# Kernel tuning notes

Hardware: AMD Instinct MI355X
Metric: run time of the kernel (lower is better)

Reference implementation:

```python
import jax, jax.numpy as jnp
import numpy as np

N, E = 50000, 800000
IN_DIM, OUT_DIM, EDGE_DIM = 128, 128, 6
LN_EPS = 1e-5


def setup_inputs() -> dict:
    key = jax.random.key(0)
    ks = jax.random.split(key, 9)
    w = lambda k, sh: (jax.random.normal(k, sh, jnp.float32) * 0.05)
    return {
        "x": jax.random.normal(ks[0], (N, IN_DIM), jnp.float32),
        "edge_attr": jax.random.normal(ks[1], (E, EDGE_DIM), jnp.float32),
        "Wn": w(ks[2], (IN_DIM, OUT_DIM)),
        "bn": jnp.zeros((OUT_DIM,), jnp.float32),
        "We": w(ks[3], (EDGE_DIM, OUT_DIM)),
        "be": jnp.zeros((OUT_DIM,), jnp.float32),
        "Wm": w(ks[4], (2 * OUT_DIM, OUT_DIM)),
        "bm": jnp.zeros((OUT_DIM,), jnp.float32),
        "gamma": jnp.ones((OUT_DIM,), jnp.float32),
        "beta": jnp.zeros((OUT_DIM,), jnp.float32),
        "edge_index": jax.random.randint(ks[5], (2, E), 0, N, jnp.int32),
    }


def reference(x, edge_attr, Wn, bn, We, be, Wm, bm, gamma, beta, edge_index):
    row, col = edge_index[0], edge_index[1]
    x_t = x @ Wn + bn                                  # [N, D]
    e_t = edge_attr @ We + be                          # [E, D]
    msgs = jnp.concatenate([x_t[col], e_t], axis=-1)   # gather + concat [E, 2D]
    msgs = jax.nn.relu(msgs @ Wm + bm)                 # [E, D]
    agg = jax.ops.segment_sum(msgs, row, num_segments=N)            # scatter_add
    deg = jax.ops.segment_sum(jnp.ones((E,), jnp.float32), row, num_segments=N)
    out = agg / jnp.clip(deg, 1.0)[:, None] + x_t      # mean-normalize + residual
    mu = out.mean(axis=-1, keepdims=True)
    var = out.var(axis=-1, keepdims=True)
    return (out - mu) * jax.lax.rsqrt(var + LN_EPS) * gamma + beta
```

## Files before the change

kernel.cpp:

```cpp
#include <hip/hip_runtime.h>
#include <hip/hip_bf16.h>

#define D 128
#define EDGE_DIM 6
#define LN_EPS 1e-5f
#define HIST_BLOCKS 2048

typedef __attribute__((ext_vector_type(8))) short short8;
typedef __attribute__((ext_vector_type(4))) float f32x4;
typedef __attribute__((ext_vector_type(2))) float f32x2;

static __device__ __forceinline__ float bf_lo(unsigned u) { return __uint_as_float(u << 16); }
static __device__ __forceinline__ float bf_hi(unsigned u) { return __uint_as_float(u & 0xffff0000u); }
static __device__ __forceinline__ unsigned short f2bf(float f) {
    __hip_bfloat16 h = __float2bfloat16(f);
    return *reinterpret_cast<unsigned short*>(&h);
}
static __device__ __forceinline__ unsigned f2fp8(float f) {
    unsigned u;
    asm("v_cvt_pk_fp8_f32 %0, %1, %2" : "=v"(u) : "v"(f), "v"(0.0f));
    return u & 0xffu;
}
static __device__ __forceinline__ f32x2 cvt2_fp8v(unsigned w) {
    f32x2 r;
    asm("v_cvt_pk_f32_fp8 %0, %1" : "=v"(r) : "v"(w));
    return r;
}

__global__ __launch_bounds__(128)
void setup_all(const float* __restrict__ Wn, const float* __restrict__ bn,
               const float* __restrict__ We, const float* __restrict__ be,
               const float* __restrict__ Wm, const float* __restrict__ bm,
               const int* __restrict__ ei, int E,
               float* __restrict__ Wnm, float* __restrict__ bnm,
               float* __restrict__ Wc, float* __restrict__ bc,
               int* __restrict__ cnt) {
    const int b = blockIdx.x;
    const int d = threadIdx.x;
    if (b < 128) {
        float acc = 0.f;
#pragma unroll 8
        for (int j = 0; j < D; ++j)
            acc = fmaf(Wn[b * D + j], Wm[j * D + d], acc);
        Wnm[b * D + d] = acc;
    } else if (b == 128) {
        float acc = 0.f;
#pragma unroll 8
        for (int j = 0; j < D; ++j)
            acc = fmaf(bn[j], Wm[j * D + d], acc);
        bnm[d] = acc;
    } else if (b < 135) {
        const int k = b - 129;
        float acc = 0.f;
#pragma unroll 8
        for (int j = 0; j < D; ++j)
            acc = fmaf(We[k * D + j], Wm[(D + j) * D + d], acc);
        Wc[k * D + d] = acc;
    } else if (b == 135) {
        float acc = bm[d];
#pragma unroll 8
        for (int j = 0; j < D; ++j)
            acc = fmaf(be[j], Wm[(D + j) * D + d], acc);
        bc[d] = acc;
    } else {
        for (int i = (b - 136) * 128 + d; i < E; i += HIST_BLOCKS * 128)
            atomicAdd(&cnt[ei[i]], 1);
    }
}

__global__ __launch_bounds__(1024)
void scan_pack(const int* __restrict__ cnt, int* __restrict__ start,
               int* __restrict__ cur, int* __restrict__ cursor, int n, int nscan,
               const float* __restrict__ Wn, const float* __restrict__ Wnm,
               unsigned short* __restrict__ Wb) {
    const int tid = threadIdx.x;
    if ((int)blockIdx.x >= nscan) {
        const int idx = ((int)blockIdx.x - nscan) * 1024 + tid;
        if (idx < 4096) {
            const int lane = idx & 63;
            const int s = (idx >> 6) & 3;
            const int ct = (idx >> 8) & 7;
            const int mat = idx >> 11;
            const float* W = mat ? Wnm : Wn;
            const int col = ct * 16 + (lane & 15);
            const int k0 = (lane >> 4) * 8 + 32 * s;
            short8 v;
#pragma unroll
            for (int j = 0; j < 8; ++j)
                v[j] = (short)f2bf(W[(size_t)(k0 + j) * D + col]);
            *reinterpret_cast<short8*>(Wb + (size_t)idx * 8) = v;
        }
        return;
    }
    __shared__ int wsum[16];
    __shared__ int sbase;
    const int lane = tid & 63, wid = tid >> 6;
    const int i = blockIdx.x * 1024 + tid;
    const int v = (i < n) ? cnt[i] : 0;
    int x = v;
#pragma unroll
    for (int off = 1; off < 64; off <<= 1) {
        int t = __shfl_up(x, off);
        if (lane >= off) x += t;
    }
    if (lane == 63) wsum[wid] = x;
    __syncthreads();
    if (wid == 0) {
        int w = (lane < 16) ? wsum[lane] : 0;
#pragma unroll
        for (int off = 1; off < 16; off <<= 1) {
            int t = __shfl_up(w, off);
            if (lane >= off) w += t;
        }
        if (lane < 16) wsum[lane] = w;
    }
    __syncthreads();
    const int total = wsum[15];
    if (tid == 0) sbase = atomicAdd(cursor, total);
    __syncthreads();
    const int woff = (wid > 0) ? wsum[wid - 1] : 0;
    if (i < n) {
        const int sv = sbase + woff + x - v;
        start[i] = sv;
        cur[i] = sv;
    }
}

__global__ __launch_bounds__(256)
void scat_gemm(const int* __restrict__ ei, int E, const float* __restrict__ ea,
               int* __restrict__ cur, uint4* __restrict__ rec, int nscat,
               const float* __restrict__ x, const unsigned short* __restrict__ Wb,
               const float* __restrict__ bn, const float* __restrict__ bnm,
               unsigned short* __restrict__ xtb, unsigned char* __restrict__ hb,
               int nrows) {
    __shared__ unsigned sR[2048 * 3];
    const int tid = threadIdx.x;
    if ((int)blockIdx.x < nscat) {
        const int base = blockIdx.x * 2048;
        const int nrec = min(2048, E - base);
        const float2* ea2 = reinterpret_cast<const float2*>(ea);
        for (int i = tid; i < nrec * 3; i += 256) {
            float2 p = ea2[(size_t)base * 3 + i];
            sR[i] = (unsigned)f2bf(p.x) | ((unsigned)f2bf(p.y) << 16);
        }
        __syncthreads();
        int rows[8], cols[8], pos[8];
#pragma unroll
        for (int it = 0; it < 8; ++it) {
            const int e = base + it * 256 + tid;
            const bool val = e < E;
            rows[it] = val ? ei[e] : -1;
            cols[it] = val ? ei[E + e] : 0;
        }
#pragma unroll
        for (int it = 0; it < 8; ++it)
            if (rows[it] >= 0) pos[it] = atomicAdd(&cur[rows[it]], 1);
#pragma unroll
        for (int it = 0; it < 8; ++it)
            if (rows[it] >= 0) {
                const int le = (it * 256 + tid) * 3;
                rec[pos[it]] = make_uint4((unsigned)cols[it], sR[le], sR[le + 1], sR[le + 2]);
            }
        return;
    }
    const int ntile = (nrows + 15) / 16;
    const int lane = tid & 63;
    const int wid = tid >> 6;
    const int t = ((int)blockIdx.x - nscat) * 4 + wid;
    if (t >= ntile) return;
    const int row16 = lane & 15;
    const int kgrp = lane >> 4;

    float biasA[8], biasB[8];
#pragma unroll
    for (int ct = 0; ct < 8; ++ct) {
        biasA[ct] = bn[ct * 16 + row16];
        biasB[ct] = bnm[ct * 16 + row16];
    }

    const int ra = t * 16 + row16;
    const bool rv = ra < nrows;
    short8 a[4];
#pragma unroll
    for (int s = 0; s < 4; ++s) {
        const float* xp = x + (size_t)ra * D + kgrp * 8 + 32 * s;
        float4 u0 = rv ? *reinterpret_cast<const float4*>(xp)
                       : make_float4(0.f, 0.f, 0.f, 0.f);
        float4 u1 = rv ? *reinterpret_cast<const float4*>(xp + 4)
                       : make_float4(0.f, 0.f, 0.f, 0.f);
        a[s][0] = (short)f2bf(u0.x); a[s][1] = (short)f2bf(u0.y);
        a[s][2] = (short)f2bf(u0.z); a[s][3] = (short)f2bf(u0.w);
        a[s][4] = (short)f2bf(u1.x); a[s][5] = (short)f2bf(u1.y);
        a[s][6] = (short)f2bf(u1.z); a[s][7] = (short)f2bf(u1.w);
    }
    const int rw0 = t * 16 + kgrp * 4;
#pragma unroll
    for (int mat = 0; mat < 2; ++mat) {
#pragma unroll
        for (int ct = 0; ct < 8; ++ct) {
            f32x4 acc = {0.f, 0.f, 0.f, 0.f};
#pragma unroll
            for (int s = 0; s < 4; ++s) {
                short8 bfr = *reinterpret_cast<const short8*>(
                    Wb + (size_t)((((mat * 8 + ct) * 4 + s) * 64 + lane)) * 8);
                acc = __builtin_amdgcn_mfma_f32_16x16x32_bf16(a[s], bfr, acc, 0, 0, 0);
            }
            const float bsc = mat ? biasB[ct] : biasA[ct];
            const int dcol = ct * 16 + row16;
#pragma unroll
            for (int j = 0; j < 4; ++j) {
                const int r = rw0 + j;
                if (r < nrows) {
                    if (mat == 0)
                        xtb[(size_t)r * D + dcol] = f2bf(acc[j] + bsc);
                    else
                        hb[(size_t)r * D + dcol] = (unsigned char)f2fp8(acc[j] + bsc);
                }
            }
        }
    }
}

__global__ __launch_bounds__(256)
void aggregate_ln(const unsigned char* __restrict__ h8,
                  const int* __restrict__ start, const int* __restrict__ cnt,
                  const uint4* __restrict__ rec,
                  const float* __restrict__ Wc, const float* __restrict__ bc,
                  const unsigned* __restrict__ xtb,
                  const float* __restrict__ gamma, const float* __restrict__ beta,
                  float* __restrict__ out, int nnode) {
    const int lane = threadIdx.x & 63;
    const int wid = threadIdx.x >> 6;

    f32x2 wc[EDGE_DIM];
#pragma unroll
    for (int k = 0; k < EDGE_DIM; ++k)
        wc[k] = reinterpret_cast<const f32x2*>(Wc)[k * 64 + lane];
    const f32x2 bc2 = reinterpret_cast<const f32x2*>(bc)[lane];
    const f32x2 g = reinterpret_cast<const f32x2*>(gamma)[lane];
    const f32x2 bb = reinterpret_cast<const f32x2*>(beta)[lane];

    for (int n = blockIdx.x * 4 + wid; n < nnode; n += gridDim.x * 4) {
        const int s = start[n];
        const int c = cnt[n];
        const unsigned xu = xtb[(unsigned)(n * 64 + lane)];
        f32x2 axy = {0.f, 0.f};
        for (int ibase = 0; ibase < c; ibase += 64) {
            const int m = min(64, c - ibase);
            uint4 rc = make_uint4(0, 0, 0, 0);
            if (lane < m) rc = rec[(size_t)(s + ibase) + lane];
            auto LDH = [&](int j) -> unsigned {
                const int jc = min(j, m - 1);
                const unsigned colj = (unsigned)__builtin_amdgcn_readlane((int)rc.x, jc);
                const unsigned short* hrow =
                    reinterpret_cast<const unsigned short*>(h8 + ((size_t)colj << 7));
                return hrow[lane];
            };
            auto COMP = [&](int j, unsigned hv) {
                const unsigned b01 = (unsigned)__builtin_amdgcn_readlane((int)rc.y, j);
                const unsigned b23 = (unsigned)__builtin_amdgcn_readlane((int)rc.z, j);
                const unsigned b45 = (unsigned)__builtin_amdgcn_readlane((int)rc.w, j);
                f32x2 e01, e23, e45, mA, mB;
                e01[0] = bf_lo(b01); e01[1] = bf_hi(b01);
                e23[0] = bf_lo(b23); e23[1] = bf_hi(b23);
                e45[0] = bf_lo(b45); e45[1] = bf_hi(b45);
                const f32x2 hx = cvt2_fp8v(hv);
                asm("v_pk_add_f32 %0, %1, %2" : "=v"(mA) : "v"(bc2), "v"(hx));
                asm("v_pk_mul_f32 %0, %1, %2 op_sel:[1,0] op_sel_hi:[1,1]"
                    : "=v"(mB) : "s"(e01), "v"(wc[1]));
                asm("v_pk_fma_f32 %0, %1, %2, %0 op_sel:[0,0,0] op_sel_hi:[0,1,1]"
                    : "+v"(mA) : "s"(e01), "v"(wc[0]));
                asm("v_pk_fma_f32 %0, %1, %2, %0 op_sel:[1,0,0] op_sel_hi:[1,1,1]"
                    : "+v"(mB) : "s"(e23), "v"(wc[3]));
                asm("v_pk_fma_f32 %0, %1, %2, %0 op_sel:[0,0,0] op_sel_hi:[0,1,1]"
                    : "+v"(mA) : "s"(e23), "v"(wc[2]));
                asm("v_pk_fma_f32 %0, %1, %2, %0 op_sel:[1,0,0] op_sel_hi:[1,1,1]"
                    : "+v"(mB) : "s"(e45), "v"(wc[5]));
                asm("v_pk_fma_f32 %0, %1, %2, %0 op_sel:[0,0,0] op_sel_hi:[0,1,1]"
                    : "+v"(mA) : "s"(e45), "v"(wc[4]));
                asm("v_pk_add_f32 %0, %0, %1" : "+v"(mA) : "v"(mB));
                axy[0] += fmaxf(mA[0], 0.f);
                axy[1] += fmaxf(mA[1], 0.f);
            };
            unsigned h0 = LDH(0), h1 = LDH(1), h2 = LDH(2), h3 = LDH(3),
                     h4 = LDH(4), h5 = LDH(5), h6 = LDH(6), h7 = LDH(7);
            int i = 0;
            for (; i + 8 <= m; i += 8) {
                COMP(i + 0, h0); h0 = LDH(i + 8);
                COMP(i + 1, h1); h1 = LDH(i + 9);
                COMP(i + 2, h2); h2 = LDH(i + 10);
                COMP(i + 3, h3); h3 = LDH(i + 11);
                COMP(i + 4, h4); h4 = LDH(i + 12);
                COMP(i + 5, h5); h5 = LDH(i + 13);
                COMP(i + 6, h6); h6 = LDH(i + 14);
                COMP(i + 7, h7); h7 = LDH(i + 15);
            }
            if (i + 0 < m) COMP(i + 0, h0);
            if (i + 1 < m) COMP(i + 1, h1);
            if (i + 2 < m) COMP(i + 2, h2);
            if (i + 3 < m) COMP(i + 3, h3);
            if (i + 4 < m) COMP(i + 4, h4);
            if (i + 5 < m) COMP(i + 5, h5);
            if (i + 6 < m) COMP(i + 6, h6);
        }
        const float inv = 1.0f / fmaxf((float)c, 1.0f);
        float o0 = fmaf(axy[0], inv, bf_lo(xu));
        float o1 = fmaf(axy[1], inv, bf_hi(xu));
        float s1 = o0 + o1, s2 = o0 * o0 + o1 * o1;
#pragma unroll
        for (int off = 32; off; off >>= 1) {
            s1 += __shfl_xor(s1, off);
            s2 += __shfl_xor(s2, off);
        }
        const float mean = s1 * (1.0f / D);
        const float var = s2 * (1.0f / D) - mean * mean;
        const float rstd = rsqrtf(var + LN_EPS);
        float2 r;
        r.x = (o0 - mean) * rstd * g[0] + bb[0];
        r.y = (o1 - mean) * rstd * g[1] + bb[1];
        reinterpret_cast<float2*>(out)[(size_t)n * 64 + lane] = r;
    }
}

extern "C" void kernel_launch(void* const* d_in, const int* in_sizes, int n_in,
                              void* d_out, int out_size, void* d_ws, size_t ws_size,
                              hipStream_t stream) {
    const float* x     = (const float*)d_in[0];
    const float* eattr = (const float*)d_in[1];
    const float* Wn    = (const float*)d_in[2];
    const float* bn    = (const float*)d_in[3];
    const float* We    = (const float*)d_in[4];
    const float* be    = (const float*)d_in[5];
    const float* Wm    = (const float*)d_in[6];
    const float* bm    = (const float*)d_in[7];
    const float* gamma = (const float*)d_in[8];
    const float* beta  = (const float*)d_in[9];
    const int*   ei    = (const int*)d_in[10];

    const int N = in_sizes[0] / D;
    const int E = in_sizes[10] / 2;

    char* ws = (char*)d_ws;
    unsigned short* xtb = (unsigned short*)ws; ws += (size_t)N * D * 2;
    unsigned char*  hb  = (unsigned char*)ws;  ws += (size_t)N * D;
    int* ints = (int*)ws;                      ws += (size_t)(N + 4) * 4;
    int* cnt = ints;
    int* cursor = ints + N;
    int* cur    = (int*)ws;                    ws += (size_t)N * 4;
    int* startv = (int*)ws;                    ws += (size_t)N * 4;
    uint4* rec  = (uint4*)ws;                  ws += (size_t)E * 16;
    float* Wnm  = (float*)ws;                  ws += (size_t)D * D * 4;
    float* bnm  = (float*)ws;                  ws += (size_t)D * 4;
    float* Wc   = (float*)ws;                  ws += (size_t)EDGE_DIM * D * 4;
    float* bcv  = (float*)ws;                  ws += (size_t)D * 4;
    unsigned short* Wb = (unsigned short*)ws;  ws += (size_t)4096 * 8 * 2;

    const int nscan = (N + 1023) / 1024;
    const int nscat = (E + 2047) / 2048;
    const int ntile = (N + 15) / 16;

    hipMemsetAsync(ints, 0, (size_t)(N + 4) * 4, stream);

    setup_all<<<136 + HIST_BLOCKS, 128, 0, stream>>>(Wn, bn, We, be, Wm, bm, ei, E,
                                                     Wnm, bnm, Wc, bcv, cnt);
    scan_pack<<<nscan + 4, 1024, 0, stream>>>(cnt, startv, cur, cursor, N, nscan,
                                              Wn, Wnm, Wb);
    scat_gemm<<<nscat + (ntile + 3) / 4, 256, 0, stream>>>(ei, E, eattr, cur, rec, nscat,
                                                           x, Wb, bn, bnm, xtb, hb, N);
    aggregate_ln<<<(N + 3) / 4, 256, 0, stream>>>(hb, startv, cnt, rec,
                                                  Wc, bcv, (const unsigned*)xtb,
                                                  gamma, beta, (float*)d_out, N);
}
```

Before: 167.5 us.

## Replace per-node global atomic scatter with two-pass bucketed counting sort

The edge scatter into CSR order changes from one global atomic per edge on per-node cursors into a two-level sort. Edges are first binned into 512-node buckets using shared-memory histograms and one global atomic per bucket per block, and written to a temporary buffer placed in the output memory. A new resort kernel then stages each bucket in LDS and scatters records to their final per-node positions. The aim is fewer global atomics and more local writes, at the cost of an extra kernel launch and an extra pass over the record array.

```diff
diff --git a/kernel.cpp b/kernel.cpp
--- a/kernel.cpp
+++ b/kernel.cpp
@@ -5,6 +5,9 @@
 #define EDGE_DIM 6
 #define LN_EPS 1e-5f
 #define HIST_BLOCKS 2048
+#define BINE 2048
+#define CB 512
+#define NB2 98
 
 typedef __attribute__((ext_vector_type(8))) short short8;
 typedef __attribute__((ext_vector_type(4))) float f32x4;
@@ -70,7 +73,7 @@
 
 __global__ __launch_bounds__(1024)
 void scan_pack(const int* __restrict__ cnt, int* __restrict__ start,
-               int* __restrict__ cur, int* __restrict__ cursor, int n, int nscan,
+               int* __restrict__ cur2, int* __restrict__ cursor, int n, int nscan,
                const float* __restrict__ Wn, const float* __restrict__ Wnm,
                unsigned short* __restrict__ Wb) {
     const int tid = threadIdx.x;
@@ -122,29 +125,31 @@
     if (i < n) {
         const int sv = sbase + woff + x - v;
         start[i] = sv;
-        cur[i] = sv;
+        if ((i & (CB - 1)) == 0) cur2[i >> 9] = sv;
     }
 }
 
 __global__ __launch_bounds__(256)
 void scat_gemm(const int* __restrict__ ei, int E, const float* __restrict__ ea,
-               int* __restrict__ cur, uint4* __restrict__ rec, int nscat,
+               int* __restrict__ cur2, uint4* __restrict__ tmp, int nbin,
                const float* __restrict__ x, const unsigned short* __restrict__ Wb,
                const float* __restrict__ bn, const float* __restrict__ bnm,
                unsigned short* __restrict__ xtb, unsigned char* __restrict__ hb,
                int nrows) {
-    __shared__ unsigned sR[2048 * 3];
+    __shared__ unsigned sR[BINE * 3];
+    __shared__ int hist[NB2];
+    __shared__ int cbase[NB2];
     const int tid = threadIdx.x;
-    if ((int)blockIdx.x < nscat) {
-        const int base = blockIdx.x * 2048;
-        const int nrec = min(2048, E - base);
+    if ((int)blockIdx.x < nbin) {
+        const int base = blockIdx.x * BINE;
+        const int nrec = min(BINE, E - base);
+        if (tid < NB2) hist[tid] = 0;
         const float2* ea2 = reinterpret_cast<const float2*>(ea);
         for (int i = tid; i < nrec * 3; i += 256) {
             float2 p = ea2[(size_t)base * 3 + i];
             sR[i] = (unsigned)f2bf(p.x) | ((unsigned)f2bf(p.y) << 16);
         }
-        __syncthreads();
-        int rows[8], cols[8], pos[8];
+        int rows[8], cols[8];
 #pragma unroll
         for (int it = 0; it < 8; ++it) {
             const int e = base + it * 256 + tid;
@@ -152,21 +157,33 @@
             rows[it] = val ? ei[e] : -1;
             cols[it] = val ? ei[E + e] : 0;
         }
+        __syncthreads();
 #pragma unroll
         for (int it = 0; it < 8; ++it)
-            if (rows[it] >= 0) pos[it] = atomicAdd(&cur[rows[it]], 1);
+            if (rows[it] >= 0) atomicAdd(&hist[rows[it] >> 9], 1);
+        __syncthreads();
+        if (tid < NB2) {
+            const int hv = hist[tid];
+            cbase[tid] = hv ? atomicAdd(&cur2[tid], hv) : 0;
+            hist[tid] = 0;
+        }
+        __syncthreads();
 #pragma unroll
         for (int it = 0; it < 8; ++it)
             if (rows[it] >= 0) {
+                const int bkt = rows[it] >> 9;
+                const int lp = atomicAdd(&hist[bkt], 1);
+                const int pos = cbase[bkt] + lp;
                 const int le = (it * 256 + tid) * 3;
-                rec[pos[it]] = make_uint4((unsigned)cols[it], sR[le], sR[le + 1], sR[le + 2]);
+                const unsigned w0 = (unsigned)cols[it] | ((unsigned)(rows[it] & (CB - 1)) << 16);
+                tmp[pos] = make_uint4(w0, sR[le], sR[le + 1], sR[le + 2]);
             }
         return;
     }
     const int ntile = (nrows + 15) / 16;
     const int lane = tid & 63;
     const int wid = tid >> 6;
-    const int t = ((int)blockIdx.x - nscat) * 4 + wid;
+    const int t = ((int)blockIdx.x - nbin) * 4 + wid;
     if (t >= ntile) return;
     const int row16 = lane & 15;
     const int kgrp = lane >> 4;
@@ -177,7 +194,6 @@
         biasA[ct] = bn[ct * 16 + row16];
         biasB[ct] = bnm[ct * 16 + row16];
     }
-
     const int ra = t * 16 + row16;
     const bool rv = ra < nrows;
     short8 a[4];
@@ -218,6 +234,35 @@
                 }
             }
         }
+    }
+}
+
+__global__ __launch_bounds__(512)
+void resort(const uint4* __restrict__ tmp, const int* __restrict__ start,
+            const int* __restrict__ cnt, uint4* __restrict__ rec, int nnode) {
+    __shared__ uint4 sRec[2048];
+    __shared__ int ncur[CB];
+    const int tid = threadIdx.x;
+    const int b = blockIdx.x;
+    const int nodes0 = b * CB;
+    const int nn = min(CB, nnode - nodes0);
+    if (tid < CB) ncur[tid] = (tid < nn) ? start[nodes0 + tid] : 0;
+    __syncthreads();
+    const int s0 = start[nodes0];
+    const int lastn = nodes0 + nn - 1;
+    const int count = start[lastn] + cnt[lastn] - s0;
+    for (int base = 0; base < count; base += 2048) {
+        const int m = min(2048, count - base);
+        for (int i = tid; i < m; i += 512)
+            sRec[i] = tmp[(size_t)(s0 + base) + i];
+        __syncthreads();
+        for (int i = tid; i < m; i += 512) {
+            const uint4 rd = sRec[i];
+            const int rl = (rd.x >> 16) & (CB - 1);
+            const int pos = atomicAdd(&ncur[rl], 1);
+            rec[pos] = make_uint4(rd.x & 0xffffu, rd.y, rd.z, rd.w);
+        }
+        __syncthreads();
     }
 }
 
@@ -339,6 +384,7 @@
 
     const int N = in_sizes[0] / D;
     const int E = in_sizes[10] / 2;
+    const int nbuck2 = (N + CB - 1) / CB;
 
     char* ws = (char*)d_ws;
     unsigned short* xtb = (unsigned short*)ws; ws += (size_t)N * D * 2;
@@ -346,7 +392,7 @@
     int* ints = (int*)ws;                      ws += (size_t)(N + 4) * 4;
     int* cnt = ints;
     int* cursor = ints + N;
-    int* cur    = (int*)ws;                    ws += (size_t)N * 4;
+    int* cur2   = (int*)ws;                    ws += (size_t)(nbuck2 + 1) * 4;
     int* startv = (int*)ws;                    ws += (size_t)N * 4;
     uint4* rec  = (uint4*)ws;                  ws += (size_t)E * 16;
     float* Wnm  = (float*)ws;                  ws += (size_t)D * D * 4;
@@ -355,18 +401,21 @@
     float* bcv  = (float*)ws;                  ws += (size_t)D * 4;
     unsigned short* Wb = (unsigned short*)ws;  ws += (size_t)4096 * 8 * 2;
 
+    uint4* tmp = (uint4*)d_out;
+
     const int nscan = (N + 1023) / 1024;
-    const int nscat = (E + 2047) / 2048;
+    const int nbin = (E + BINE - 1) / BINE;
     const int ntile = (N + 15) / 16;
 
     hipMemsetAsync(ints, 0, (size_t)(N + 4) * 4, stream);
 
     setup_all<<<136 + HIST_BLOCKS, 128, 0, stream>>>(Wn, bn, We, be, Wm, bm, ei, E,
                                                      Wnm, bnm, Wc, bcv, cnt);
-    scan_pack<<<nscan + 4, 1024, 0, stream>>>(cnt, startv, cur, cursor, N, nscan,
+    scan_pack<<<nscan + 4, 1024, 0, stream>>>(cnt, startv, cur2, cursor, N, nscan,
                                               Wn, Wnm, Wb);
-    scat_gemm<<<nscat + (ntile + 3) / 4, 256, 0, stream>>>(ei, E, eattr, cur, rec, nscat,
-                                                           x, Wb, bn, bnm, xtb, hb, N);
+    scat_gemm<<<nbin + (ntile + 3) / 4, 256, 0, stream>>>(ei, E, eattr, cur2, tmp, nbin,
+                                                          x, Wb, bn, bnm, xtb, hb, N);
+    resort<<<nbuck2, 512, 0, stream>>>(tmp, startv, cnt, rec, N);
     aggregate_ln<<<(N + 3) / 4, 256, 0, stream>>>(hb, startv, cnt, rec,
                                                   Wc, bcv, (const unsigned*)xtb,
                                                   gamma, beta, (float*)d_out, N);
```

Measured after the change: 152.4 us. -9.0%, faster.
